# Kernel tuning notes

Measured on AMD Instinct MI355X. Metric: run time of the kernel, lower is better.

Reference implementation:

```python
import jax, jax.numpy as jnp
import numpy as np

B, S, H, K, V = 1024, 50, 128, 4, 100000
ROUTING_TIMES = 3

def _squash(c):
    # c: [B,K,1,H]
    cap_norm = jnp.sum(jnp.square(c), -1, keepdims=True)
    scalar_factor = cap_norm / (1.0 + cap_norm) / jnp.sqrt(cap_norm + 1e-9)
    return scalar_factor * c

def setup_inputs() -> dict:
    key = jax.random.key(0)
    k1, k2, k3, k4, k5, k6 = jax.random.split(key, 6)
    item_seq = jax.random.randint(k1, (B, S), 0, V)
    mask = jax.random.randint(k2, (B, S), 0, 2).astype(jnp.float32)
    item = jax.random.randint(k3, (B, 1), 0, V)
    emb = jax.random.normal(k4, (V, H), dtype=jnp.float32) * 0.02
    W = jax.random.normal(k5, (H, H), dtype=jnp.float32) * (1.0 / np.sqrt(H))
    # bilinear_type==0 -> capsule routing logits initialized with randn
    capsule_weight0 = jax.random.normal(k6, (B, K, S), dtype=jnp.float32)
    return {"item_seq": item_seq, "mask": mask, "item": item,
            "emb": emb, "W": W, "capsule_weight0": capsule_weight0}

def reference(item_seq, mask, item, emb, W, capsule_weight0):
    # padding_idx=0: lookups see a zeroed row 0 (and get no grad there),
    # but calculate_loss uses the raw weight matrix.
    emb_lookup = emb.at[0].set(0.0)
    seq_emb = emb_lookup[item_seq]          # [B,S,H]
    item_e = emb_lookup[item[:, 0]]         # [B,H]  (squeeze(1))

    # CapsuleNetwork, bilinear_type==0: Linear(H,H,no bias) then repeat_interleave along hidden
    h = seq_emb @ W.T                        # [B,S,H]
    hat = jnp.repeat(h, K, axis=2)           # [B,S,H*K] (repeat_interleave semantics)
    hat = hat.reshape(B, S, K, H).transpose(0, 2, 1, 3)  # [B,K,S,H]
    hat_iter = jax.lax.stop_gradient(hat)    # stop_grad=True (detach)

    atten_mask = jnp.broadcast_to(mask[:, None, :], (B, K, S))
    cw = capsule_weight0
    cap = None
    for i in range(ROUTING_TIMES):
        # torch F.softmax with no dim on a 3-D tensor uses dim=0 (batch axis) -- faithful
        sw = jax.nn.softmax(cw, axis=0)
        sw = jnp.where(atten_mask == 0, 0.0, sw)[:, :, None, :]  # [B,K,1,S]
        src = hat_iter if i < ROUTING_TIMES - 1 else hat
        cap = _squash(sw @ src)                                   # [B,K,1,H]
        if i < ROUTING_TIMES - 1:
            delta = (hat_iter @ jnp.swapaxes(cap, 3, 2)).reshape(B, K, S)
            cw = cw + delta

    user_emb = cap.reshape(B, K, H)          # multi_interest_emb

    # hard readout: pick interest with max dot against target item
    cos = jnp.einsum('bkh,bh->bk', user_emb, item_e)
    k_index = jnp.argmax(cos, axis=1)        # [B]
    best = jnp.take_along_axis(user_emb, k_index[:, None, None], axis=1)[:, 0]  # [B,H]

    # cross-entropy over all items (raw embedding weight)
    scores = best @ emb.T                    # [B,V]
    logp = jax.nn.log_softmax(scores, axis=-1)
    loss = -jnp.mean(jnp.take_along_axis(logp, item, axis=1))
    return user_emb, loss
```

## Files before the change

kernel.cpp:

```cpp
#include <hip/hip_runtime.h>
#include <math.h>

#define BB 1024
#define SS 50
#define SSP 51
#define HH 128
#define KK 4
#define VV 100000
#define NVT 782
#define NVT8 784
#define VPAD (NVT8*128)
#define KS (KK*SS)
#define NHM 400
#define NPAD_ALL 352.0f
#define CONVB 2048
#define LOG2E 1.44269504f

#define SVPB 7
#define SNCH 14
#define SGRID (8*8*SNCH)

typedef __attribute__((ext_vector_type(8))) short bf16x8;
typedef __attribute__((ext_vector_type(4))) float f32x4;

__device__ __forceinline__ ushort f2bf(float x) {
  unsigned u = __float_as_uint(x);
  unsigned r = u + 0x7FFF + ((u >> 16) & 1);
  return (ushort)(r >> 16);
}
__device__ __forceinline__ float bf2f(ushort u) {
  return __uint_as_float(((unsigned)u) << 16);
}
__device__ __forceinline__ bf16x8 cvt8(float4 a, float4 b) {
  bf16x8 r;
  r[0] = (short)f2bf(a.x); r[1] = (short)f2bf(a.y);
  r[2] = (short)f2bf(a.z); r[3] = (short)f2bf(a.w);
  r[4] = (short)f2bf(b.x); r[5] = (short)f2bf(b.y);
  r[6] = (short)f2bf(b.z); r[7] = (short)f2bf(b.w);
  return r;
}

__global__ __launch_bounds__(256) void k_pre(const float* __restrict__ emb,
                                             const float* __restrict__ cw0,
                                             float* __restrict__ cm,
                                             float* __restrict__ s1,
                                             float* __restrict__ s2,
                                             float* __restrict__ accum,
                                             const int* __restrict__ item_seq,
                                             const float* __restrict__ W,
                                             ushort* __restrict__ hb16,
                                             ushort* __restrict__ embb) {
  const int t = threadIdx.x;
  if (blockIdx.x < NHM) {
    __shared__ __align__(16) ushort sWf[32 * 512];
    const int w = t >> 6;
    const int lane = t & 63;
    const int lr = lane & 15;
    const int lq = lane >> 4;
    const int m0 = blockIdx.x * 128;

#pragma unroll
    for (int it = 0; it < 8; ++it) {
      int pos = t + it * 256;
      int ch = pos >> 6, l = pos & 63;
      int n = (ch & 7) * 16 + (l & 15);
      int k0 = (ch >> 3) * 32 + (l >> 4) * 8;
      float4 a = *(const float4*)&W[n * HH + k0];
      float4 b = *(const float4*)&W[n * HH + k0 + 4];
      *(bf16x8*)&sWf[ch * 512 + l * 8] = cvt8(a, b);
    }

    bf16x8 af[4][2];
#pragma unroll
    for (int vv = 0; vv < 2; ++vv) {
      int m = m0 + w * 32 + vv * 16 + lr;
      int idx = item_seq[m];
#pragma unroll
      for (int ks = 0; ks < 4; ++ks) {
        if (idx != 0) {
          float4 a = *(const float4*)&emb[(size_t)idx * HH + ks * 32 + lq * 8];
          float4 b = *(const float4*)&emb[(size_t)idx * HH + ks * 32 + lq * 8 + 4];
          af[ks][vv] = cvt8(a, b);
        } else {
          af[ks][vv] = (bf16x8){0, 0, 0, 0, 0, 0, 0, 0};
        }
      }
    }
    __syncthreads();

    f32x4 acc[8][2];
#pragma unroll
    for (int nt = 0; nt < 8; ++nt)
#pragma unroll
      for (int vv = 0; vv < 2; ++vv) acc[nt][vv] = (f32x4){0.f, 0.f, 0.f, 0.f};

#pragma unroll
    for (int ks = 0; ks < 4; ++ks) {
      bf16x8 bw[8];
#pragma unroll
      for (int nt = 0; nt < 8; ++nt)
        bw[nt] = *(const bf16x8*)&sWf[(ks * 8 + nt) * 512 + lane * 8];
#pragma unroll
      for (int nt = 0; nt < 8; ++nt)
#pragma unroll
        for (int vv = 0; vv < 2; ++vv)
          acc[nt][vv] = __builtin_amdgcn_mfma_f32_16x16x32_bf16(af[ks][vv], bw[nt], acc[nt][vv], 0, 0, 0);
    }

#pragma unroll
    for (int nt = 0; nt < 8; ++nt)
#pragma unroll
      for (int vv = 0; vv < 2; ++vv)
#pragma unroll
        for (int r = 0; r < 4; ++r) {
          int m = m0 + w * 32 + vv * 16 + lq * 4 + r;
          hb16[(size_t)m * HH + nt * 16 + lr] = f2bf(acc[nt][vv][r]);
        }
  } else if (blockIdx.x < NHM + KS) {
    __shared__ float red[256];
    const int c = blockIdx.x - NHM;
    if (t < 8) s1[t * KS + c] = 0.f;
    if (t >= 8 && t < 16) s2[(t - 8) * KS + c] = 0.f;
    if (c < 4) accum[c * 256 + t] = 0.f;
    float s = 0.f;
    for (int b = t; b < BB; b += 256) s += __expf(cw0[(size_t)b * KS + c]);
    red[t] = s;
    __syncthreads();
    for (int o = 128; o > 0; o >>= 1) {
      if (t < o) red[t] += red[t + o];
      __syncthreads();
    }
    if (t == 0) cm[c] = red[0];
  } else {
    const size_t stride = (size_t)CONVB * 256 * 4;
    for (size_t i = ((size_t)(blockIdx.x - NHM - KS) * 256 + t) * 4;
         i < (size_t)VPAD * HH; i += stride) {
      ushort4 o;
      if (i < (size_t)VV * HH) {
        float4 v = *(const float4*)&emb[i];
        o = make_ushort4(f2bf(v.x), f2bf(v.y), f2bf(v.z), f2bf(v.w));
      } else {
        o = make_ushort4(0, 0, 0, 0);
      }
      *(ushort4*)&embb[i] = o;
    }
  }
}

__global__ __launch_bounds__(256) void k_route(const float* __restrict__ cwsrc,
                                               float* __restrict__ cwdst,
                                               const ushort* __restrict__ hb16,
                                               const float* __restrict__ csum,
                                               int nslots,
                                               const float* __restrict__ mask,
                                               int last,
                                               float* __restrict__ out_ue,
                                               const float* __restrict__ emb,
                                               const int* __restrict__ item,
                                               ushort* __restrict__ bestb,
                                               float* __restrict__ csnext,
                                               float* __restrict__ si) {
  __shared__ ushort shT[128 * SSP];
  __shared__ float swl[KS];
  __shared__ float c32p[256];
  __shared__ float c32[128];
  __shared__ float csq[128];
  __shared__ float ie4r[32];
  __shared__ float ie4z[32];
  __shared__ float fac[4];
  __shared__ float cosk[4];
  __shared__ float cosr[4];
  __shared__ int kb;
  const int t = threadIdx.x;
  const int b = blockIdx.x;

  for (int p = t; p < (SS * HH) / 4; p += 256) {
    int flat = 4 * p;
    int s = flat >> 7, col = flat & 127;
    ushort4 v = *(const ushort4*)&hb16[(size_t)b * SS * HH + flat];
    shT[(col + 0) * SSP + s] = v.x;
    shT[(col + 1) * SSP + s] = v.y;
    shT[(col + 2) * SSP + s] = v.z;
    shT[(col + 3) * SSP + s] = v.w;
  }
  if (t < KS) {
    float den = 0.f;
    for (int g2 = 0; g2 < nslots; ++g2) den += csum[g2 * KS + t];
    float v = __expf(cwsrc[(size_t)b * KS + t]) / den;
    if (mask[b * SS + (t % SS)] == 0.0f) v = 0.0f;
    swl[t] = v;
  }
  __syncthreads();

  {
    int col = t & 127;
    int half = t >> 7;
    int k = col >> 5;
    float acc = 0.f;
    const float* swk = &swl[k * SS + half * 25];
    const ushort* hc = &shT[col * SSP + half * 25];
    for (int s = 0; s < 25; ++s) acc += swk[s] * bf2f(hc[s]);
    c32p[t] = acc;
  }
  __syncthreads();
  if (t < 128) c32[t] = c32p[t] + c32p[t + 128];
  __syncthreads();
  if (t < 4) {
    float nrm = 0.f;
#pragma unroll
    for (int j = 0; j < 32; ++j) { float c = c32[32 * t + j]; nrm += c * c; }
    nrm *= 4.0f;
    fac[t] = nrm / (1.0f + nrm) / sqrtf(nrm + 1e-9f);
  }
  __syncthreads();
  if (t < 128) csq[t] = c32[t] * fac[t >> 5];
  __syncthreads();

  if (!last) {
    if (t < KS) {
      int k = t / SS, s = t % SS;
      const float* cq = &csq[32 * k];
      float d = 0.f;
#pragma unroll
      for (int j = 0; j < 32; ++j) d += bf2f(shT[(32 * k + j) * SSP + s]) * cq[j];
      float nv = cwsrc[(size_t)b * KS + t] + 4.0f * d;
      cwdst[(size_t)b * KS + t] = nv;
      atomicAdd(&csnext[(b & 7) * KS + t], __expf(nv));
    }
  } else {
    for (int hh = t; hh < 512; hh += 256) {
      int k = hh >> 7, r = (hh & 127) >> 2;
      out_ue[(size_t)b * 512 + hh] = csq[32 * k + r];
    }
    if (t < 32) {
      int idx = item[b];
      const float* e = emb + (size_t)idx * HH + 4 * t;
      float v = e[0] + e[1] + e[2] + e[3];
      ie4r[t] = v;
      ie4z[t] = (idx == 0) ? 0.f : v;
    }
    __syncthreads();
    if (t < 4) {
      float cz = 0.f, cr = 0.f;
#pragma unroll
      for (int j = 0; j < 32; ++j) {
        cz += csq[32 * t + j] * ie4z[j];
        cr += csq[32 * t + j] * ie4r[j];
      }
      cosk[t] = cz; cosr[t] = cr;
    }
    __syncthreads();
    if (t == 0) {
      int kbest = 0; float bv = cosk[0];
#pragma unroll
      for (int k = 1; k < 4; ++k) if (cosk[k] > bv) { bv = cosk[k]; kbest = k; }
      kb = kbest;
      si[b] = cosr[kbest];
    }
    __syncthreads();
    if (t < 128) bestb[(size_t)b * HH + t] = f2bf(csq[32 * kb + (t >> 2)] * LOG2E);
  }
}

__global__ __launch_bounds__(256) void k_score_mfma(const ushort* __restrict__ bestb,
                                                    const ushort* __restrict__ embb,
                                                    float* __restrict__ accum) {
  const int lin = blockIdx.x;
  const int xcd = lin & 7;
  const int j = lin >> 3;
  const int bt8 = j & 7;
  const int chunk = j >> 3;
  const int vt0 = xcd * 98 + chunk * SVPB;

  __shared__ float ssm[128][2];
  const int t = threadIdx.x;
  const int w = t >> 6;
  const int lane = t & 63;
  const int lr = lane & 15;
  const int lq = lane >> 4;
  const int wv = w >> 1;
  const int wb = w & 1;
  const int b0 = bt8 * 128 + wb * 64;

  bf16x8 bf[4][4];
#pragma unroll
  for (int ks = 0; ks < 4; ++ks)
#pragma unroll
    for (int bt = 0; bt < 4; ++bt)
      bf[ks][bt] = *(const bf16x8*)&bestb[(size_t)(b0 + bt * 16 + lr) * HH + ks * 32 + lq * 8];

  const ushort* pv[4];
#pragma unroll
  for (int vv = 0; vv < 4; ++vv)
    pv[vv] = &embb[(size_t)(vt0 * 128 + wv * 64 + vv * 16 + lr) * HH + lq * 8];

  float sacc[4] = {0.f, 0.f, 0.f, 0.f};

  for (int i = 0; i < SVPB; ++i) {
    bf16x8 af[4][4];
#pragma unroll
    for (int vv = 0; vv < 4; ++vv)
#pragma unroll
      for (int ks = 0; ks < 4; ++ks)
        af[ks][vv] = *(const bf16x8*)&pv[vv][ks * 32];

    f32x4 acc[4][4];
#pragma unroll
    for (int bt = 0; bt < 4; ++bt)
#pragma unroll
      for (int vv = 0; vv < 4; ++vv) acc[bt][vv] = (f32x4){0.f, 0.f, 0.f, 0.f};

#pragma unroll
    for (int ks = 0; ks < 4; ++ks)
#pragma unroll
      for (int bt = 0; bt < 4; ++bt)
#pragma unroll
        for (int vv = 0; vv < 4; ++vv)
          acc[bt][vv] = __builtin_amdgcn_mfma_f32_16x16x32_bf16(af[ks][vv], bf[ks][bt], acc[bt][vv], 0, 0, 0);

#pragma unroll
    for (int bt = 0; bt < 4; ++bt) {
      float s = 0.f;
#pragma unroll
      for (int vv = 0; vv < 4; ++vv)
#pragma unroll
        for (int r = 0; r < 4; ++r) s += exp2f(acc[bt][vv][r]);
      sacc[bt] += s;
    }
#pragma unroll
    for (int vv = 0; vv < 4; ++vv) pv[vv] += 128 * HH;
  }

#pragma unroll
  for (int bt = 0; bt < 4; ++bt) {
    float s = sacc[bt];
    s += __shfl_xor(s, 16);
    s += __shfl_xor(s, 32);
    if (lq == 0) ssm[wb * 64 + bt * 16 + lr][wv] = s;
  }
  __syncthreads();
  if (t < 128) atomicAdd(&accum[bt8 * 128 + t], ssm[t][0] + ssm[t][1]);
}

__global__ __launch_bounds__(256) void k_loss(const float* __restrict__ accum,
                                              const float* __restrict__ si,
                                              float* __restrict__ outloss) {
  __shared__ float red[256];
  const int t = threadIdx.x;
  float s = 0.f;
  for (int b = t; b < BB; b += 256)
    s += logf(accum[b] - NPAD_ALL) - si[b];
  red[t] = s;
  __syncthreads();
  for (int o = 128; o > 0; o >>= 1) {
    if (t < o) red[t] += red[t + o];
    __syncthreads();
  }
  if (t == 0) outloss[0] = red[0] / (float)BB;
}

extern "C" void kernel_launch(void* const* d_in, const int* in_sizes, int n_in,
                              void* d_out, int out_size, void* d_ws, size_t ws_size,
                              hipStream_t stream) {
  const int*   item_seq = (const int*)d_in[0];
  const float* mask     = (const float*)d_in[1];
  const int*   item     = (const int*)d_in[2];
  const float* emb      = (const float*)d_in[3];
  const float* W        = (const float*)d_in[4];
  const float* cw0      = (const float*)d_in[5];
  float* out = (float*)d_out;
  float* outloss = out + (size_t)BB * KK * HH;

  float* ws = (float*)d_ws;
  float* cm    = ws;
  float* s1    = cm + 256;
  float* s2    = s1 + 8 * KS;
  float* si    = s2 + 8 * KS;
  float* accum = si + BB;
  float* cw    = accum + BB;
  ushort* hb16  = (ushort*)(cw + (size_t)BB * KS);
  ushort* embb  = hb16 + (size_t)BB * SS * HH;
  ushort* bestb = embb + (size_t)VPAD * HH;

  k_pre<<<dim3(NHM + KS + CONVB), 256, 0, stream>>>(emb, cw0, cm, s1, s2, accum,
                                                    item_seq, W, hb16, embb);

  k_route<<<dim3(BB), 256, 0, stream>>>(cw0, cw, hb16, cm, 1, mask, 0, out, emb, item, bestb, s1, si);
  k_route<<<dim3(BB), 256, 0, stream>>>(cw, cw, hb16, s1, 8, mask, 0, out, emb, item, bestb, s2, si);
  k_route<<<dim3(BB), 256, 0, stream>>>(cw, cw, hb16, s2, 8, mask, 1, out, emb, item, bestb, s1, si);

  k_score_mfma<<<dim3(SGRID), 256, 0, stream>>>(bestb, embb, accum);
  k_loss<<<dim3(1), 256, 0, stream>>>(accum, si, outloss);
}
```

Before: 216.2 us.

## Give each score block one vocab tile and use fast exp2 intrinsic

The score kernel no longer loops over seven vocabulary tiles per block. Each block now handles a single 128-row tile, so the grid grows to NVT8*8 blocks. The accumulators are computed one batch sub-tile at a time, which cuts live registers, and the exponentials use the raw __builtin_amdgcn_exp2f plus a tree reduction. The aim is more parallelism and occupancy with less register pressure, at the cost of more blocks, more atomics, and reloading the bestb fragments per tile.

```diff
diff --git a/kernel.cpp b/kernel.cpp
--- a/kernel.cpp
+++ b/kernel.cpp
@@ -15,10 +15,7 @@
 #define NPAD_ALL 352.0f
 #define CONVB 2048
 #define LOG2E 1.44269504f
-
-#define SVPB 7
-#define SNCH 14
-#define SGRID (8*8*SNCH)
+#define SGRID (NVT8*8)
 
 typedef __attribute__((ext_vector_type(8))) short bf16x8;
 typedef __attribute__((ext_vector_type(4))) float f32x4;
@@ -267,10 +264,9 @@
                                                     float* __restrict__ accum) {
   const int lin = blockIdx.x;
   const int xcd = lin & 7;
-  const int j = lin >> 3;
-  const int bt8 = j & 7;
-  const int chunk = j >> 3;
-  const int vt0 = xcd * 98 + chunk * SVPB;
+  const int g = lin >> 3;
+  const int bt8 = g & 7;
+  const int vt = xcd * 98 + (g >> 3);
 
   __shared__ float ssm[128][2];
   const int t = threadIdx.x;
@@ -281,6 +277,14 @@
   const int wv = w >> 1;
   const int wb = w & 1;
   const int b0 = bt8 * 128 + wb * 64;
+  const int v0 = vt * 128 + wv * 64;
+
+  bf16x8 af[4][4];
+#pragma unroll
+  for (int vv = 0; vv < 4; ++vv)
+#pragma unroll
+    for (int ks = 0; ks < 4; ++ks)
+      af[ks][vv] = *(const bf16x8*)&embb[(size_t)(v0 + vv * 16 + lr) * HH + ks * 32 + lq * 8];
 
   bf16x8 bf[4][4];
 #pragma unroll
@@ -289,46 +293,30 @@
     for (int bt = 0; bt < 4; ++bt)
       bf[ks][bt] = *(const bf16x8*)&bestb[(size_t)(b0 + bt * 16 + lr) * HH + ks * 32 + lq * 8];
 
-  const ushort* pv[4];
-#pragma unroll
-  for (int vv = 0; vv < 4; ++vv)
-    pv[vv] = &embb[(size_t)(vt0 * 128 + wv * 64 + vv * 16 + lr) * HH + lq * 8];
-
-  float sacc[4] = {0.f, 0.f, 0.f, 0.f};
-
-  for (int i = 0; i < SVPB; ++i) {
-    bf16x8 af[4][4];
+  float sacc[4];
+#pragma unroll
+  for (int bt = 0; bt < 4; ++bt) {
+    f32x4 acc[4];
+#pragma unroll
+    for (int vv = 0; vv < 4; ++vv) acc[vv] = (f32x4){0.f, 0.f, 0.f, 0.f};
+#pragma unroll
+    for (int ks = 0; ks < 4; ++ks)
+#pragma unroll
+      for (int vv = 0; vv < 4; ++vv)
+        acc[vv] = __builtin_amdgcn_mfma_f32_16x16x32_bf16(af[ks][vv], bf[ks][bt], acc[vv], 0, 0, 0);
+
+    float e[16];
 #pragma unroll
     for (int vv = 0; vv < 4; ++vv)
 #pragma unroll
-      for (int ks = 0; ks < 4; ++ks)
-        af[ks][vv] = *(const bf16x8*)&pv[vv][ks * 32];
-
-    f32x4 acc[4][4];
-#pragma unroll
-    for (int bt = 0; bt < 4; ++bt)
-#pragma unroll
-      for (int vv = 0; vv < 4; ++vv) acc[bt][vv] = (f32x4){0.f, 0.f, 0.f, 0.f};
-
-#pragma unroll
-    for (int ks = 0; ks < 4; ++ks)
-#pragma unroll
-      for (int bt = 0; bt < 4; ++bt)
-#pragma unroll
-        for (int vv = 0; vv < 4; ++vv)
-          acc[bt][vv] = __builtin_amdgcn_mfma_f32_16x16x32_bf16(af[ks][vv], bf[ks][bt], acc[bt][vv], 0, 0, 0);
-
-#pragma unroll
-    for (int bt = 0; bt < 4; ++bt) {
-      float s = 0.f;
-#pragma unroll
-      for (int vv = 0; vv < 4; ++vv)
-#pragma unroll
-        for (int r = 0; r < 4; ++r) s += exp2f(acc[bt][vv][r]);
-      sacc[bt] += s;
-    }
-#pragma unroll
-    for (int vv = 0; vv < 4; ++vv) pv[vv] += 128 * HH;
+      for (int r = 0; r < 4; ++r)
+        e[vv * 4 + r] = __builtin_amdgcn_exp2f(acc[vv][r]);
+#pragma unroll
+    for (int o = 8; o > 0; o >>= 1)
+#pragma unroll
+      for (int i = 0; i < 16; ++i)
+        if (i < o) e[i] += e[i + o];
+    sacc[bt] = e[0];
   }
 
 #pragma unroll
```

New measurement: 236.8 us. +9.5%, slower.
